# Optimization experiments

Measured on AMD Instinct MI355X. Metric: run time of the kernel, lower is better.

The kernel has to match this reference:

```python
import jax, jax.numpy as jnp
import numpy as np

D = 256      # model dim
H = 4        # heads
L = 6        # layers (shared weights)
N = 32768    # neuron dim; per-head hidden = N//H = 8192
VOCAB = 256
B, T = 2, 2048
EPS = 1e-5


def _ln(x):
    # LayerNorm over last dim, no affine (matches nn.LayerNorm(D, elementwise_affine=False))
    m = jnp.mean(x, axis=-1, keepdims=True)
    v = jnp.mean((x - m) ** 2, axis=-1, keepdims=True)
    return (x - m) * jax.lax.rsqrt(v + EPS)


def _rope(x):
    # x: [B, H, T, d]
    d = x.shape[-1]
    t = x.shape[-2]
    inv_freq = 1.0 / (10000.0 ** (jnp.arange(0, d, 2, dtype=jnp.float32) / d))
    freqs = jnp.arange(t, dtype=jnp.float32)[:, None] * inv_freq[None, :]  # [T, d/2]
    emb = jnp.concatenate([freqs, freqs], axis=-1)                          # [T, d]
    x1, x2 = x[..., : d // 2], x[..., d // 2 :]
    x_rot = jnp.concatenate([-x2, x1], axis=-1)
    return x * jnp.cos(emb) + x_rot * jnp.sin(emb)


def _linear_attn(q, k, v):
    # q,k: [B,H,T,n]; v: [B,T,D]. Raw (unnormalized) scores, STRICTLY causal mask
    # (tril with diagonal=-1, i.e. token t attends to s < t only), no softmax.
    qr = _rope(q)
    kr = _rope(k)
    scores = jnp.einsum('bhtn,bhsn->bhts', qr, kr)  # [B,H,T,T]
    t_idx = jnp.arange(q.shape[-2])
    mask = t_idx[:, None] > t_idx[None, :]          # strict lower triangle
    scores = jnp.where(mask, scores, jnp.zeros((), scores.dtype))
    return jnp.einsum('bhts,bsd->bhtd', scores, v)  # [B,H,T,D]


def setup_inputs() -> dict:
    key = jax.random.key(0)
    ks = jax.random.split(key, 6)
    idx = jax.random.randint(ks[0], (B, T), 0, VOCAB, dtype=jnp.int64)
    std = 0.02
    wte = std * jax.random.normal(ks[1], (VOCAB, D), dtype=jnp.float32)
    encoder = std * jax.random.normal(ks[2], (N, D), dtype=jnp.float32)
    decoder_x = std * jax.random.normal(ks[3], (H, D, N // H), dtype=jnp.float32)
    decoder_y = std * jax.random.normal(ks[4], (H, D, N // H), dtype=jnp.float32)
    readout = std * jax.random.normal(ks[5], (D, VOCAB), dtype=jnp.float32)
    return {"idx": idx, "wte": wte, "encoder": encoder,
            "decoder_x": decoder_x, "decoder_y": decoder_y, "readout": readout}


def reference(idx, wte, encoder, decoder_x, decoder_y, readout):
    # Dropout is identity in eval mode.
    v_ast = _ln(wte[idx])  # [B,T,D]
    for _ in range(L):  # weights SHARED across layers
        x = jax.nn.relu(jnp.einsum('btd,hdn->bhtn', v_ast, decoder_x))  # [B,H,T,N/H]
        a_ast = _linear_attn(x, x, v_ast)                               # [B,H,T,D]
        y = jax.nn.relu(jnp.einsum('bhtd,hdn->bhtn', _ln(a_ast), decoder_y)) * x
        y_flat = jnp.transpose(y, (0, 2, 1, 3)).reshape(y.shape[0], y.shape[2], N)  # [B,T,N]
        v_ast = _ln(v_ast + _ln(y_flat @ encoder))
    return v_ast @ readout  # [B,T,VOCAB]
```

## Files before the change

kernel.cpp:

```cpp
#include <hip/hip_runtime.h>
#include <stdint.h>

typedef unsigned short u16;
typedef __bf16 bfv8 __attribute__((ext_vector_type(8)));
typedef float f32x4 __attribute__((ext_vector_type(4)));

#define BM 128
#define BN 128
#define BK 32

__device__ __forceinline__ float b2f(u16 u){ union{float f; unsigned int i;} x; x.i = ((unsigned int)u)<<16; return x.f; }
__device__ __forceinline__ u16 f2b(float f){ union{float f; unsigned int i;} x; x.f = f; unsigned int r = x.i + 0x7fffu + ((x.i>>16)&1u); return (u16)(r>>16); }

__device__ __forceinline__ void load16_lds(const void* g, void* l){
  __builtin_amdgcn_global_load_lds(
      (const __attribute__((address_space(1))) void*)g,
      (__attribute__((address_space(3))) void*)l, 16, 0, 0);
}

__device__ __forceinline__ void swz(int& bx, int& by, int& bz){
  int gx = gridDim.x, gy = gridDim.y;
  int nw = gx*gy*gridDim.z;
  int flat = blockIdx.x + gx*(blockIdx.y + gy*blockIdx.z);
  int q = nw >> 3, r = nw & 7, xcd = flat & 7, i = flat >> 3;
  int wg = (xcd < r ? xcd*(q+1) : r*(q+1) + (xcd-r)*q) + i;
  bx = wg % gx; int t = wg / gx; by = t % gy; bz = t / gy;
}

struct GP {
  const u16* A; const u16* Bt; const u16* A2; const u16* Bt2;
  const u16* ct; const u16* st;
  float* Cf; u16* Cb; u16* Y;
  int bh0, zs, zm;
};

template<int LDA, int LDB, bool PAIRB>
__device__ __forceinline__ void kloop(const u16* A, const u16* Bt, int m0, int n0,
                                      int kbeg, int kend,
                                      u16 (&As)[2][4096], u16 (&Bs)[2][4096],
                                      f32x4 (&acc)[4][4]){
  const int tid = threadIdx.x;
  const int lane = tid & 63;
  const int wid = tid >> 6;
  const int wm = wid >> 1, wn = wid & 1;
  const int srow = tid >> 2, sslot = tid & 3;
  const int nt = (kend - kbeg) / BK;
  if (nt <= 0) return;

  auto stage = [&](int k0, int buf){
    #pragma unroll
    for (int q = 0; q < 2; ++q){
      int row = q*64 + srow;
      int ks = sslot ^ ((row >> 1) & 3);
      load16_lds(A + (long)(m0 + row)*LDA + (k0 + ks*8), &As[buf][q*2048 + wid*512]);
    }
    #pragma unroll
    for (int q = 0; q < 2; ++q){
      int row = q*64 + srow;
      int ks = sslot ^ ((row >> 1) & 3);
      long brow;
      if (PAIRB){ int wnb = row >> 6, sub = (row >> 5) & 1, r5 = row & 31;
                  brow = n0 + wnb*32 + r5 + sub*4096; }
      else brow = n0 + row;
      load16_lds(Bt + brow*(long)LDB + (k0 + ks*8), &Bs[buf][q*2048 + wid*512]);
    }
  };
  auto compute = [&](int buf){
    bfv8 af[4], bf[4];
    const int r16 = lane & 15, s4 = lane >> 4;
    #pragma unroll
    for (int i = 0; i < 4; ++i){
      int ar = wm*64 + i*16 + r16;
      af[i] = *(const bfv8*)(&As[buf][ar*BK + ((s4 ^ ((ar>>1)&3))*8)]);
      int br = wn*64 + i*16 + r16;
      bf[i] = *(const bfv8*)(&Bs[buf][br*BK + ((s4 ^ ((br>>1)&3))*8)]);
    }
    #pragma unroll
    for (int i = 0; i < 4; ++i)
      #pragma unroll
      for (int j = 0; j < 4; ++j)
        acc[i][j] = __builtin_amdgcn_mfma_f32_16x16x32_bf16(af[i], bf[j], acc[i][j], 0,0,0);
  };

  stage(kbeg, 0);
  int cur = 0;
  for (int t = 0; t < nt-1; ++t){
    stage(kbeg + (t+1)*BK, cur^1);
    asm volatile("s_waitcnt vmcnt(4)" ::: "memory");
    __builtin_amdgcn_s_barrier();
    compute(cur);
    asm volatile("s_waitcnt lgkmcnt(0)" ::: "memory");
    __builtin_amdgcn_s_barrier();
    cur ^= 1;
  }
  asm volatile("s_waitcnt vmcnt(0)" ::: "memory");
  __builtin_amdgcn_s_barrier();
  compute(cur);
  asm volatile("s_waitcnt lgkmcnt(0)" ::: "memory");
  __builtin_amdgcn_s_barrier();
}

template<int LDA, int LDB, int PAIR>
__device__ __forceinline__ void kloop256(const u16* A, const u16* Bt, int m0, int n0,
                                         int kbeg, int kend,
                                         u16 (&As)[2][8192], u16 (&Bs)[2][8192],
                                         f32x4 (&acc)[8][4]){
  const int tid = threadIdx.x;
  const int lane = tid & 63;
  const int wid = tid >> 6;
  const int srow = tid >> 2;
  const int sslot = tid & 3;
  const int nt = (kend - kbeg) / BK;
  if (nt <= 0) return;

  auto stage = [&](int k0, int buf){
    #pragma unroll
    for (int q = 0; q < 2; ++q){
      int row = q*128 + srow;
      int ks = sslot ^ ((row >> 1) & 3);
      load16_lds(A + (long)(m0 + row)*LDA + (k0 + ks*8), &As[buf][q*4096 + wid*512]);
    }
    #pragma unroll
    for (int q = 0; q < 2; ++q){
      int row = q*128 + srow;
      int ks = sslot ^ ((row >> 1) & 3);
      long brow;
      if (PAIR) brow = n0 + (row & 127) + (long)(row >> 7)*4096;
      else      brow = n0 + row;
      load16_lds(Bt + brow*(long)LDB + (k0 + ks*8), &Bs[buf][q*4096 + wid*512]);
    }
  };
  auto compute = [&](int buf){
    const int wm = wid >> 2, wn = wid & 3;
    const int r16 = lane & 15, s4 = lane >> 4;
    bfv8 af[8], bf[4];
    #pragma unroll
    for (int i = 0; i < 8; ++i){
      int ar = wm*128 + i*16 + r16;
      af[i] = *(const bfv8*)(&As[buf][ar*BK + ((s4 ^ ((ar>>1)&3))*8)]);
    }
    #pragma unroll
    for (int j = 0; j < 4; ++j){
      int br;
      if (PAIR) br = (j < 2) ? (wn*32 + j*16 + r16) : (128 + wn*32 + (j-2)*16 + r16);
      else      br = wn*64 + j*16 + r16;
      bf[j] = *(const bfv8*)(&Bs[buf][br*BK + ((s4 ^ ((br>>1)&3))*8)]);
    }
    #pragma unroll
    for (int i = 0; i < 8; ++i)
      #pragma unroll
      for (int j = 0; j < 4; ++j)
        acc[i][j] = __builtin_amdgcn_mfma_f32_16x16x32_bf16(af[i], bf[j], acc[i][j], 0,0,0);
  };

  stage(kbeg, 0);
  int cur = 0;
  for (int t = 0; t < nt-1; ++t){
    stage(kbeg + (t+1)*BK, cur^1);
    asm volatile("s_waitcnt vmcnt(4)" ::: "memory");
    __builtin_amdgcn_s_barrier();
    compute(cur);
    asm volatile("s_waitcnt lgkmcnt(0)" ::: "memory");
    __builtin_amdgcn_s_barrier();
    cur ^= 1;
  }
  asm volatile("s_waitcnt vmcnt(0)" ::: "memory");
  __builtin_amdgcn_s_barrier();
  compute(cur);
  asm volatile("s_waitcnt lgkmcnt(0)" ::: "memory");
  __builtin_amdgcn_s_barrier();
}

#define EPI_SETUP const int lane = threadIdx.x & 63, wid = threadIdx.x >> 6; \
  const int wm = wid >> 1, wn = wid & 1; const int r16 = lane & 15, s4 = lane >> 4;
#define EPI_SETUP8 const int lane = threadIdx.x & 63, wid = threadIdx.x >> 6; \
  const int wm = wid >> 2, wn = wid & 3; const int r16 = lane & 15, s4 = lane >> 4;

__global__ __launch_bounds__(512) void g_rope(GP p){
  int bx, by, bz; swz(bx, by, bz);
  const int m0 = by*256, n0 = bx*128, z = bz;
  const int bh = p.bh0 + z, b = bh >> 2, h = bh & 3;
  __shared__ u16 As[2][8192], Bs[2][8192];
  f32x4 acc[8][4] = {};
  kloop256<256,256,1>(p.A + (long)b*524288, p.Bt + (long)h*2097152, m0, n0, 0, 256, As, Bs, acc);
  EPI_SETUP8
  #pragma unroll
  for (int i = 0; i < 8; ++i)
    #pragma unroll
    for (int j = 0; j < 2; ++j){
      int cl = n0 + wn*32 + j*16 + r16;
      #pragma unroll
      for (int v = 0; v < 4; ++v){
        int row = m0 + wm*128 + i*16 + s4*4 + v;
        float x1 = fmaxf(acc[i][j][v], 0.f);
        float x2 = fmaxf(acc[i][j+2][v], 0.f);
        float c = b2f(p.ct[(long)row*4096 + cl]);
        float s = b2f(p.st[(long)row*4096 + cl]);
        p.Cb[(long)z*16777216 + (long)row*8192 + cl]        = f2b(x1*c - x2*s);
        p.Cb[(long)z*16777216 + (long)row*8192 + cl + 4096] = f2b(x2*c + x1*s);
      }
    }
}

__global__ __launch_bounds__(512) void g_qk(GP p){
  int bx, by, bz; swz(bx, by, bz);
  const int m0 = by*256, n0 = bx*256, z = bz;
  if (n0 > m0) return;
  __shared__ u16 As[2][8192], Bs[2][8192];
  f32x4 acc[8][4] = {};
  const u16* A = p.A + (long)z*16777216;
  kloop256<8192,8192,0>(A, A, m0, n0, 0, 8192, As, Bs, acc);
  EPI_SETUP8
  u16* C = p.Cb + (long)z*4194304;
  #pragma unroll
  for (int i = 0; i < 8; ++i)
    #pragma unroll
    for (int j = 0; j < 4; ++j){
      int col = n0 + wn*64 + j*16 + r16;
      #pragma unroll
      for (int v = 0; v < 4; ++v){
        int row = m0 + wm*128 + i*16 + s4*4 + v;
        C[(long)row*2048 + col] = f2b(row > col ? acc[i][j][v] : 0.f);
      }
    }
}

__global__ __launch_bounds__(512) void g_enc(GP p){
  int bx, by, bz; swz(bx, by, bz);
  const int m0 = by*256, sp = bx, head = bz;
  const int h = (p.bh0 + head) & 3;
  const int kbeg = sp*4096, kend = kbeg + 4096;
  __shared__ u16 As[2][8192], Bs[2][8192];
  f32x4 acc[8][4] = {};
  kloop256<8192,32768,0>(p.A + (long)head*16777216, p.Bt + (long)h*8192, m0, 0, kbeg, kend, As, Bs, acc);
  EPI_SETUP8
  float* C = p.Cf + (long)(head*2 + sp)*524288;
  #pragma unroll
  for (int i = 0; i < 8; ++i)
    #pragma unroll
    for (int j = 0; j < 4; ++j){
      int col = wn*64 + j*16 + r16;
      #pragma unroll
      for (int v = 0; v < 4; ++v){
        int row = m0 + wm*128 + i*16 + s4*4 + v;
        C[(long)row*256 + col] = acc[i][j][v];
      }
    }
}

__global__ __launch_bounds__(256) void g_pv(GP p){
  int bx, by, bz; swz(bx, by, bz);
  const int m0 = by*BM, n0 = bx*BN;
  const int head = bz >> p.zs, sl = bz & p.zm;
  const int b = (p.bh0 + head) >> 2;
  const int kc = 2048 >> p.zs;
  const int kbeg = sl*kc;
  const int kend = min(min(2048, m0 + BM), kbeg + kc);
  __shared__ u16 As[2][4096], Bs[2][4096];
  f32x4 acc[4][4] = {};
  kloop<2048,2048,false>(p.A + (long)head*4194304, p.Bt + (long)b*524288, m0, n0, kbeg, kend, As, Bs, acc);
  EPI_SETUP
  #pragma unroll
  for (int i = 0; i < 4; ++i)
    #pragma unroll
    for (int j = 0; j < 4; ++j){
      int col = n0 + wn*64 + j*16 + r16;
      #pragma unroll
      for (int v = 0; v < 4; ++v){
        int row = m0 + wm*64 + i*16 + s4*4 + v;
        p.Cf[(long)bz*524288 + (long)row*256 + col] = acc[i][j][v];
      }
    }
}

__global__ __launch_bounds__(256) void g_fuse(GP p){
  int bx, by, bz; swz(bx, by, bz);
  const int m0 = by*BM, n0 = bx*BN, z = bz;
  const int bh = p.bh0 + z, b = bh >> 2, h = bh & 3;
  __shared__ u16 As[2][4096], Bs[2][4096];
  f32x4 acc1[4][4] = {}, acc2[4][4] = {};
  kloop<256,256,false>(p.A  + (long)z*524288, p.Bt  + (long)h*2097152, m0, n0, 0, 256, As, Bs, acc1);
  kloop<256,256,false>(p.A2 + (long)b*524288, p.Bt2 + (long)h*2097152, m0, n0, 0, 256, As, Bs, acc2);
  EPI_SETUP
  #pragma unroll
  for (int i = 0; i < 4; ++i)
    #pragma unroll
    for (int j = 0; j < 4; ++j){
      int col = n0 + wn*64 + j*16 + r16;
      #pragma unroll
      for (int v = 0; v < 4; ++v){
        int row = m0 + wm*64 + i*16 + s4*4 + v;
        p.Y[(long)z*16777216 + (long)row*8192 + col] =
            f2b(fmaxf(acc1[i][j][v], 0.f) * fmaxf(acc2[i][j][v], 0.f));
      }
    }
}

__global__ __launch_bounds__(256) void g_out(GP p){
  int bx, by, bz; swz(bx, by, bz); (void)bz;
  const int m0 = by*BM, n0 = bx*BN;
  __shared__ u16 As[2][4096], Bs[2][4096];
  f32x4 acc[4][4] = {};
  kloop<256,256,false>(p.A, p.Bt, m0, n0, 0, 256, As, Bs, acc);
  EPI_SETUP
  #pragma unroll
  for (int i = 0; i < 4; ++i)
    #pragma unroll
    for (int j = 0; j < 4; ++j){
      int col = n0 + wn*64 + j*16 + r16;
      #pragma unroll
      for (int v = 0; v < 4; ++v){
        int row = m0 + wm*64 + i*16 + s4*4 + v;
        p.Cf[(long)row*256 + col] = acc[i][j][v];
      }
    }
}


__device__ __forceinline__ float wave_sum(float v){
  #pragma unroll
  for (int o = 32; o > 0; o >>= 1) v += __shfl_down(v, o, 64);
  return v;
}
__device__ __forceinline__ float block_sum(float v, float* sm){
  v = wave_sum(v);
  __syncthreads();
  if ((threadIdx.x & 63) == 0) sm[threadIdx.x >> 6] = v;
  __syncthreads();
  return sm[0] + sm[1] + sm[2] + sm[3];
}

__global__ __launch_bounds__(256) void k_embed(const int* idx, const float* wte,
                                               u16* vbf, u16* vbt){
  __shared__ float sm[4];
  __shared__ int is64_s;
  int row = blockIdx.x, d = threadIdx.x;
  int oddnz = (d < 64) ? (idx[2*d + 1] != 0) : 0;
  unsigned long long mb = __ballot(oddnz);
  if (threadIdx.x == 0) is64_s = (mb == 0ULL);
  __syncthreads();
  int tok = is64_s ? idx[2*row] : idx[row];
  float x = wte[tok*256 + d];
  float m = block_sum(x, sm) * (1.f/256.f);
  float dd = x - m;
  float var = block_sum(dd*dd, sm) * (1.f/256.f);
  float y = dd * rsqrtf(var + 1e-5f);
  vbf[(long)row*256 + d] = f2b(y);
  int b = row >> 11, t = row & 2047;
  vbt[((long)(b*256 + d))*2048 + t] = f2b(y);
}

__global__ __launch_bounds__(256) void k_ln(const float* abuf, u16* out, int pv){
  __shared__ float sm[4];
  int row = blockIdx.x, d = threadIdx.x;
  int head = row >> 11, t = row & 2047;
  float x = 0.f;
  for (int s = 0; s < pv; ++s) x += abuf[((long)(head*pv + s) << 19) + (long)t*256 + d];
  float m = block_sum(x, sm) * (1.f/256.f);
  float dd = x - m;
  float var = block_sum(dd*dd, sm) * (1.f/256.f);
  out[(long)row*256 + d] = f2b(dd * rsqrtf(var + 1e-5f));
}

__global__ __launch_bounds__(256) void k_acc(const float* part, float* t1,
                                             int bh0, int gc, int ps){
  int t = blockIdx.x, d = threadIdx.x;
  long o = (long)t*256 + d;
  float s0 = 0.f, s1 = 0.f;
  for (int z = 0; z < gc; ++z){
    float v = 0.f;
    for (int sp = 0; sp < ps; ++sp) v += part[((long)(z*ps + sp) << 19) + o];
    if (((bh0 + z) >> 2) == 0) s0 += v; else s1 += v;
  }
  #pragma unroll
  for (int b = 0; b < 2; ++b){
    int lo = bh0 > 4*b ? bh0 : 4*b;
    int hi = (bh0 + gc) < (4*b + 4) ? (bh0 + gc) : (4*b + 4);
    if (lo < hi){
      float s = b == 0 ? s0 : s1;
      if (lo == 4*b) t1[((long)b << 19) + o] = s;
      else           t1[((long)b << 19) + o] += s;
    }
  }
}

__global__ __launch_bounds__(256) void k_finish(const float* t1, u16* vbf, u16* vbt){
  __shared__ float sm[4];
  int row = blockIdx.x; int d = threadIdx.x;
  int b = row >> 11, t = row & 2047;
  float s = t1[(long)row*256 + d];
  float m = block_sum(s, sm) * (1.f/256.f);
  float dd = s - m;
  float var = block_sum(dd*dd, sm) * (1.f/256.f);
  float u = dd * rsqrtf(var + 1e-5f);
  float wv = b2f(vbf[(long)row*256 + d]) + u;
  float m2 = block_sum(wv, sm) * (1.f/256.f);
  float d2 = wv - m2;
  float v2 = block_sum(d2*d2, sm) * (1.f/256.f);
  float y = d2 * rsqrtf(v2 + 1e-5f);
  vbf[(long)row*256 + d] = f2b(y);
  vbt[((long)(b*256 + d))*2048 + t] = f2b(y);
}

__global__ __launch_bounds__(256) void k_cossin(u16* ct, u16* st){
  int tid = blockIdx.x*256 + threadIdx.x;
  int t = tid >> 12, i = tid & 4095;
  float f = powf(10000.0f, -(float)i * (1.0f/4096.0f));
  float a = (float)t * f;
  float s, c; sincosf(a, &s, &c);
  ct[tid] = f2b(c); st[tid] = f2b(s);
}

__global__ void k_transpose(const float* in, u16* out, int R, int C, long in_z, long out_z){
  __shared__ float tile[32][33];
  const float* I = in + (long)blockIdx.z * in_z;
  u16* O = out + (long)blockIdx.z * out_z;
  int c0 = blockIdx.x*32, r0 = blockIdx.y*32;
  int tx = threadIdx.x, ty = threadIdx.y;
  #pragma unroll
  for (int k = 0; k < 4; ++k){ int r = ty + k*8; tile[r][tx] = I[(long)(r0+r)*C + c0+tx]; }
  __syncthreads();
  #pragma unroll
  for (int k = 0; k < 4; ++k){ int r = ty + k*8; O[(long)(c0+r)*R + r0+tx] = f2b(tile[tx][r]); }
}


extern "C" void kernel_launch(void* const* d_in, const int* in_sizes, int n_in,
                              void* d_out, int out_size, void* d_ws, size_t ws_size,
                              hipStream_t stream){
  const int*   idx = (const int*)d_in[0];
  const float* wte = (const float*)d_in[1];
  const float* enc = (const float*)d_in[2];
  const float* dx  = (const float*)d_in[3];
  const float* dy  = (const float*)d_in[4];
  const float* ro  = (const float*)d_in[5];
  float* out = (float*)d_out;
  (void)in_sizes; (void)n_in; (void)out_size;

  int gc = 1, pv = 2;
  {
    const int gcs[4] = {4, 3, 2, 1};
    for (int i = 0; i < 4; ++i){
      int g = gcs[i]; int pvt = (g >= 4) ? 1 : 2;
      size_t need = 92274688UL + (size_t)g*(33554432UL + 8388608UL + (size_t)pvt*2097152UL);
      if (need <= ws_size){ gc = g; pv = pvt; break; }
    }
  }
  const int ps = 2;
  const int pvs = (pv == 2) ? 1 : 0;

  char* w = (char*)d_ws;
  size_t off = 0;
  auto alloc = [&](size_t b){ size_t r = off; off += (b + 255) & ~(size_t)255; return r; };
  u16*   v_bf  = (u16*)  (w + alloc(4096UL*256*2));
  u16*   v_bt  = (u16*)  (w + alloc(2UL*256*2048*2));
  u16*   dxT   = (u16*)  (w + alloc(4UL*8192*256*2));
  u16*   dyT   = (u16*)  (w + alloc(4UL*8192*256*2));
  u16*   encT  = (u16*)  (w + alloc(256UL*32768*2));
  u16*   ct    = (u16*)  (w + alloc(2048UL*4096*2));
  u16*   st    = (u16*)  (w + alloc(2048UL*4096*2));
  float* t1    = (float*)(w + alloc(2UL*2048*256*4));
  u16*   xbuf  = (u16*)  (w + alloc((size_t)gc*33554432));
  u16*   scb   = (u16*)  (w + alloc((size_t)gc*8388608));
  float* abuf  = (float*)(w + alloc((size_t)gc*pv*2097152UL));
  float* part  = (float*)scb;
  u16*   lnAb  = (u16*)((char*)scb + (size_t)gc*ps*2097152UL);
  u16*   roT   = (u16*)t1;

  dim3 tb(32, 8);
  k_cossin<<<32768, 256, 0, stream>>>(ct, st);
  k_transpose<<<dim3(256, 8, 4),  tb, 0, stream>>>(dx,  dxT,  256,   8192, 256L*8192, 8192L*256);
  k_transpose<<<dim3(256, 8, 4),  tb, 0, stream>>>(dy,  dyT,  256,   8192, 256L*8192, 8192L*256);
  k_transpose<<<dim3(8, 1024, 1), tb, 0, stream>>>(enc, encT, 32768, 256,  0, 0);
  k_embed<<<4096, 256, 0, stream>>>(idx, wte, v_bf, v_bt);

  for (int l = 0; l < 6; ++l){
    for (int bh0 = 0; bh0 < 8; bh0 += gc){
      int ze = (8 - bh0 < gc) ? (8 - bh0) : gc;
      { GP g{}; g.bh0=bh0; g.A=v_bf; g.Bt=dxT; g.ct=ct; g.st=st; g.Cb=xbuf;
        g_rope<<<dim3(32,8,ze), 512, 0, stream>>>(g); }
      { GP g{}; g.bh0=bh0; g.A=xbuf; g.Cb=scb;
        g_qk<<<dim3(8,8,ze), 512, 0, stream>>>(g); }
      { GP g{}; g.bh0=bh0; g.A=scb; g.Bt=v_bt; g.Cf=abuf; g.zs=pvs; g.zm=pv-1;
        g_pv<<<dim3(2,16,ze*pv), 256, 0, stream>>>(g); }
      k_ln<<<ze*2048, 256, 0, stream>>>(abuf, lnAb, pv);
      { GP g{}; g.bh0=bh0; g.A=lnAb; g.Bt=dyT; g.A2=v_bf; g.Bt2=dxT; g.Y=xbuf;
        g_fuse<<<dim3(64,16,ze), 256, 0, stream>>>(g); }
      { GP g{}; g.bh0=bh0; g.A=xbuf; g.Bt=encT; g.Cf=part;
        g_enc<<<dim3(ps,8,ze), 512, 0, stream>>>(g); }
      k_acc<<<2048, 256, 0, stream>>>(part, t1, bh0, ze, ps);
    }
    k_finish<<<4096, 256, 0, stream>>>(t1, v_bf, v_bt);
  }
  k_transpose<<<dim3(8, 8, 1), tb, 0, stream>>>(ro, roT, 256, 256, 0, 0);
  { GP g{}; g.A=v_bf; g.Bt=roT; g.Cf=out;
    g_out<<<dim3(2,32,1), 256, 0, stream>>>(g); }
}
```

Before: 8.809 ms.

## Retile GEMM kernels: BK=64 for 128-tiles, 256-tile fuse, 128-tile qk/enc

After: 8.659 ms. Within noise of the previous version (-1.7%).

```diff
diff --git a/kernel.cpp b/kernel.cpp
--- a/kernel.cpp
+++ b/kernel.cpp
@@ -7,7 +7,7 @@
 
 #define BM 128
 #define BN 128
-#define BK 32
+#define BK 64
 
 __device__ __forceinline__ float b2f(u16 u){ union{float f; unsigned int i;} x; x.i = ((unsigned int)u)<<16; return x.f; }
 __device__ __forceinline__ u16 f2b(float f){ union{float f; unsigned int i;} x; x.f = f; unsigned int r = x.i + 0x7fffu + ((x.i>>16)&1u); return (u16)(r>>16); }
@@ -37,27 +37,28 @@
 template<int LDA, int LDB, bool PAIRB>
 __device__ __forceinline__ void kloop(const u16* A, const u16* Bt, int m0, int n0,
                                       int kbeg, int kend,
-                                      u16 (&As)[2][4096], u16 (&Bs)[2][4096],
+                                      u16 (&As)[2][8192], u16 (&Bs)[2][8192],
                                       f32x4 (&acc)[4][4]){
   const int tid = threadIdx.x;
   const int lane = tid & 63;
   const int wid = tid >> 6;
   const int wm = wid >> 1, wn = wid & 1;
-  const int srow = tid >> 2, sslot = tid & 3;
+  const int rr = tid >> 3;
+  const int slot = tid & 7;
   const int nt = (kend - kbeg) / BK;
   if (nt <= 0) return;
 
   auto stage = [&](int k0, int buf){
     #pragma unroll
-    for (int q = 0; q < 2; ++q){
-      int row = q*64 + srow;
-      int ks = sslot ^ ((row >> 1) & 3);
+    for (int q = 0; q < 4; ++q){
+      int row = q*32 + rr;
+      int ks = slot ^ (row & 7);
       load16_lds(A + (long)(m0 + row)*LDA + (k0 + ks*8), &As[buf][q*2048 + wid*512]);
     }
     #pragma unroll
-    for (int q = 0; q < 2; ++q){
-      int row = q*64 + srow;
-      int ks = sslot ^ ((row >> 1) & 3);
+    for (int q = 0; q < 4; ++q){
+      int row = q*32 + rr;
+      int ks = slot ^ (row & 7);
       long brow;
       if (PAIRB){ int wnb = row >> 6, sub = (row >> 5) & 1, r5 = row & 31;
                   brow = n0 + wnb*32 + r5 + sub*4096; }
@@ -66,26 +67,100 @@
     }
   };
   auto compute = [&](int buf){
-    bfv8 af[4], bf[4];
     const int r16 = lane & 15, s4 = lane >> 4;
     #pragma unroll
-    for (int i = 0; i < 4; ++i){
-      int ar = wm*64 + i*16 + r16;
-      af[i] = *(const bfv8*)(&As[buf][ar*BK + ((s4 ^ ((ar>>1)&3))*8)]);
-      int br = wn*64 + i*16 + r16;
-      bf[i] = *(const bfv8*)(&Bs[buf][br*BK + ((s4 ^ ((br>>1)&3))*8)]);
-    }
-    #pragma unroll
-    for (int i = 0; i < 4; ++i)
-      #pragma unroll
-      for (int j = 0; j < 4; ++j)
-        acc[i][j] = __builtin_amdgcn_mfma_f32_16x16x32_bf16(af[i], bf[j], acc[i][j], 0,0,0);
+    for (int kk = 0; kk < 2; ++kk){
+      bfv8 af[4], bf[4];
+      #pragma unroll
+      for (int i = 0; i < 4; ++i){
+        int ar = wm*64 + i*16 + r16;
+        af[i] = *(const bfv8*)(&As[buf][ar*64 + (((kk*4 + s4) ^ (ar & 7))*8)]);
+        int br = wn*64 + i*16 + r16;
+        bf[i] = *(const bfv8*)(&Bs[buf][br*64 + (((kk*4 + s4) ^ (br & 7))*8)]);
+      }
+      #pragma unroll
+      for (int i = 0; i < 4; ++i)
+        #pragma unroll
+        for (int j = 0; j < 4; ++j)
+          acc[i][j] = __builtin_amdgcn_mfma_f32_16x16x32_bf16(af[i], bf[j], acc[i][j], 0,0,0);
+    }
   };
 
   stage(kbeg, 0);
   int cur = 0;
   for (int t = 0; t < nt-1; ++t){
     stage(kbeg + (t+1)*BK, cur^1);
+    asm volatile("s_waitcnt vmcnt(8)" ::: "memory");
+    __builtin_amdgcn_s_barrier();
+    compute(cur);
+    asm volatile("s_waitcnt lgkmcnt(0)" ::: "memory");
+    __builtin_amdgcn_s_barrier();
+    cur ^= 1;
+  }
+  asm volatile("s_waitcnt vmcnt(0)" ::: "memory");
+  __builtin_amdgcn_s_barrier();
+  compute(cur);
+  asm volatile("s_waitcnt lgkmcnt(0)" ::: "memory");
+  __builtin_amdgcn_s_barrier();
+}
+
+template<int LDA, int LDB, int PAIR>
+__device__ __forceinline__ void kloop256(const u16* A, const u16* Bt, int m0, int n0,
+                                         int kbeg, int kend,
+                                         u16 (&As)[2][8192], u16 (&Bs)[2][8192],
+                                         f32x4 (&acc)[8][4]){
+  const int tid = threadIdx.x;
+  const int lane = tid & 63;
+  const int wid = tid >> 6;
+  const int srow = tid >> 2;
+  const int sslot = tid & 3;
+  const int nt = (kend - kbeg) / 32;
+  if (nt <= 0) return;
+
+  auto stage = [&](int k0, int buf){
+    #pragma unroll
+    for (int q = 0; q < 2; ++q){
+      int row = q*128 + srow;
+      int ks = sslot ^ ((row >> 1) & 3);
+      load16_lds(A + (long)(m0 + row)*LDA + (k0 + ks*8), &As[buf][q*4096 + wid*512]);
+    }
+    #pragma unroll
+    for (int q = 0; q < 2; ++q){
+      int row = q*128 + srow;
+      int ks = sslot ^ ((row >> 1) & 3);
+      long brow;
+      if (PAIR) brow = n0 + (row & 127) + (long)(row >> 7)*4096;
+      else      brow = n0 + row;
+      load16_lds(Bt + brow*(long)LDB + (k0 + ks*8), &Bs[buf][q*4096 + wid*512]);
+    }
+  };
+  auto compute = [&](int buf){
+    const int wm = wid >> 2, wn = wid & 3;
+    const int r16 = lane & 15, s4 = lane >> 4;
+    bfv8 af[8], bf[4];
+    #pragma unroll
+    for (int i = 0; i < 8; ++i){
+      int ar = wm*128 + i*16 + r16;
+      af[i] = *(const bfv8*)(&As[buf][ar*32 + ((s4 ^ ((ar>>1)&3))*8)]);
+    }
+    #pragma unroll
+    for (int j = 0; j < 4; ++j){
+      int br;
+      if (PAIR) br = (j < 2) ? (wn*32 + j*16 + r16) : (128 + wn*32 + (j-2)*16 + r16);
+      else      br = wn*64 + j*16 + r16;
+      bf[j] = *(const bfv8*)(&Bs[buf][br*32 + ((s4 ^ ((br>>1)&3))*8)]);
+    }
+    #pragma unroll
+    for (int i = 0; i < 8; ++i)
+      #pragma unroll
+      for (int j = 0; j < 4; ++j)
+        acc[i][j] = __builtin_amdgcn_mfma_f32_16x16x32_bf16(af[i], bf[j], acc[i][j], 0,0,0);
+  };
+
+  stage(kbeg, 0);
+  int cur = 0;
+  for (int t = 0; t < nt-1; ++t){
+    stage(kbeg + (t+1)*32, cur^1);
     asm volatile("s_waitcnt vmcnt(4)" ::: "memory");
     __builtin_amdgcn_s_barrier();
     compute(cur);
@@ -100,77 +175,6 @@
   __builtin_amdgcn_s_barrier();
 }
 
-template<int LDA, int LDB, int PAIR>
-__device__ __forceinline__ void kloop256(const u16* A, const u16* Bt, int m0, int n0,
-                                         int kbeg, int kend,
-                                         u16 (&As)[2][8192], u16 (&Bs)[2][8192],
-                                         f32x4 (&acc)[8][4]){
-  const int tid = threadIdx.x;
-  const int lane = tid & 63;
-  const int wid = tid >> 6;
-  const int srow = tid >> 2;
-  const int sslot = tid & 3;
-  const int nt = (kend - kbeg) / BK;
-  if (nt <= 0) return;
-
-  auto stage = [&](int k0, int buf){
-    #pragma unroll
-    for (int q = 0; q < 2; ++q){
-      int row = q*128 + srow;
-      int ks = sslot ^ ((row >> 1) & 3);
-      load16_lds(A + (long)(m0 + row)*LDA + (k0 + ks*8), &As[buf][q*4096 + wid*512]);
-    }
-    #pragma unroll
-    for (int q = 0; q < 2; ++q){
-      int row = q*128 + srow;
-      int ks = sslot ^ ((row >> 1) & 3);
-      long brow;
-      if (PAIR) brow = n0 + (row & 127) + (long)(row >> 7)*4096;
-      else      brow = n0 + row;
-      load16_lds(Bt + brow*(long)LDB + (k0 + ks*8), &Bs[buf][q*4096 + wid*512]);
-    }
-  };
-  auto compute = [&](int buf){
-    const int wm = wid >> 2, wn = wid & 3;
-    const int r16 = lane & 15, s4 = lane >> 4;
-    bfv8 af[8], bf[4];
-    #pragma unroll
-    for (int i = 0; i < 8; ++i){
-      int ar = wm*128 + i*16 + r16;
-      af[i] = *(const bfv8*)(&As[buf][ar*BK + ((s4 ^ ((ar>>1)&3))*8)]);
-    }
-    #pragma unroll
-    for (int j = 0; j < 4; ++j){
-      int br;
-      if (PAIR) br = (j < 2) ? (wn*32 + j*16 + r16) : (128 + wn*32 + (j-2)*16 + r16);
-      else      br = wn*64 + j*16 + r16;
-      bf[j] = *(const bfv8*)(&Bs[buf][br*BK + ((s4 ^ ((br>>1)&3))*8)]);
-    }
-    #pragma unroll
-    for (int i = 0; i < 8; ++i)
-      #pragma unroll
-      for (int j = 0; j < 4; ++j)
-        acc[i][j] = __builtin_amdgcn_mfma_f32_16x16x32_bf16(af[i], bf[j], acc[i][j], 0,0,0);
-  };
-
-  stage(kbeg, 0);
-  int cur = 0;
-  for (int t = 0; t < nt-1; ++t){
-    stage(kbeg + (t+1)*BK, cur^1);
-    asm volatile("s_waitcnt vmcnt(4)" ::: "memory");
-    __builtin_amdgcn_s_barrier();
-    compute(cur);
-    asm volatile("s_waitcnt lgkmcnt(0)" ::: "memory");
-    __builtin_amdgcn_s_barrier();
-    cur ^= 1;
-  }
-  asm volatile("s_waitcnt vmcnt(0)" ::: "memory");
-  __builtin_amdgcn_s_barrier();
-  compute(cur);
-  asm volatile("s_waitcnt lgkmcnt(0)" ::: "memory");
-  __builtin_amdgcn_s_barrier();
-}
-
 #define EPI_SETUP const int lane = threadIdx.x & 63, wid = threadIdx.x >> 6; \
   const int wm = wid >> 1, wn = wid & 1; const int r16 = lane & 15, s4 = lane >> 4;
 #define EPI_SETUP8 const int lane = threadIdx.x & 63, wid = threadIdx.x >> 6; \
@@ -202,48 +206,25 @@
     }
 }
 
-__global__ __launch_bounds__(512) void g_qk(GP p){
+__global__ __launch_bounds__(256) void g_qk(GP p){
   int bx, by, bz; swz(bx, by, bz);
-  const int m0 = by*256, n0 = bx*256, z = bz;
-  if (n0 > m0) return;
+  const int m0 = by*BM, n0 = bx*BN, z = bz;
+  if (n0 >= m0 + BM) return;
   __shared__ u16 As[2][8192], Bs[2][8192];
-  f32x4 acc[8][4] = {};
+  f32x4 acc[4][4] = {};
   const u16* A = p.A + (long)z*16777216;
-  kloop256<8192,8192,0>(A, A, m0, n0, 0, 8192, As, Bs, acc);
-  EPI_SETUP8
+  kloop<8192,8192,false>(A, A, m0, n0, 0, 8192, As, Bs, acc);
+  EPI_SETUP
   u16* C = p.Cb + (long)z*4194304;
   #pragma unroll
-  for (int i = 0; i < 8; ++i)
+  for (int i = 0; i < 4; ++i)
     #pragma unroll
     for (int j = 0; j < 4; ++j){
       int col = n0 + wn*64 + j*16 + r16;
       #pragma unroll
       for (int v = 0; v < 4; ++v){
-        int row = m0 + wm*128 + i*16 + s4*4 + v;
+        int row = m0 + wm*64 + i*16 + s4*4 + v;
         C[(long)row*2048 + col] = f2b(row > col ? acc[i][j][v] : 0.f);
-      }
-    }
-}
-
-__global__ __launch_bounds__(512) void g_enc(GP p){
-  int bx, by, bz; swz(bx, by, bz);
-  const int m0 = by*256, sp = bx, head = bz;
-  const int h = (p.bh0 + head) & 3;
-  const int kbeg = sp*4096, kend = kbeg + 4096;
-  __shared__ u16 As[2][8192], Bs[2][8192];
-  f32x4 acc[8][4] = {};
-  kloop256<8192,32768,0>(p.A + (long)head*16777216, p.Bt + (long)h*8192, m0, 0, kbeg, kend, As, Bs, acc);
-  EPI_SETUP8
-  float* C = p.Cf + (long)(head*2 + sp)*524288;
-  #pragma unroll
-  for (int i = 0; i < 8; ++i)
-    #pragma unroll
-    for (int j = 0; j < 4; ++j){
-      int col = wn*64 + j*16 + r16;
-      #pragma unroll
-      for (int v = 0; v < 4; ++v){
-        int row = m0 + wm*128 + i*16 + s4*4 + v;
-        C[(long)row*256 + col] = acc[i][j][v];
       }
     }
 }
@@ -256,7 +237,7 @@
   const int kc = 2048 >> p.zs;
   const int kbeg = sl*kc;
   const int kend = min(min(2048, m0 + BM), kbeg + kc);
-  __shared__ u16 As[2][4096], Bs[2][4096];
+  __shared__ u16 As[2][8192], Bs[2][8192];
   f32x4 acc[4][4] = {};
   kloop<2048,2048,false>(p.A + (long)head*4194304, p.Bt + (long)b*524288, m0, n0, kbeg, kend, As, Bs, acc);
   EPI_SETUP
@@ -273,14 +254,49 @@
     }
 }
 
-__global__ __launch_bounds__(256) void g_fuse(GP p){
+__global__ __launch_bounds__(512) void g_fuse(GP p){
   int bx, by, bz; swz(bx, by, bz);
-  const int m0 = by*BM, n0 = bx*BN, z = bz;
+  const int m0 = by*256, n0 = bx*256, z = bz;
   const int bh = p.bh0 + z, b = bh >> 2, h = bh & 3;
-  __shared__ u16 As[2][4096], Bs[2][4096];
-  f32x4 acc1[4][4] = {}, acc2[4][4] = {};
-  kloop<256,256,false>(p.A  + (long)z*524288, p.Bt  + (long)h*2097152, m0, n0, 0, 256, As, Bs, acc1);
-  kloop<256,256,false>(p.A2 + (long)b*524288, p.Bt2 + (long)h*2097152, m0, n0, 0, 256, As, Bs, acc2);
+  __shared__ u16 As[2][8192], Bs[2][8192];
+  f32x4 acc[8][4] = {};
+  kloop256<256,256,0>(p.A + (long)z*524288, p.Bt + (long)h*2097152, m0, n0, 0, 256, As, Bs, acc);
+  unsigned stash[8][4][2];
+  #pragma unroll
+  for (int i = 0; i < 8; ++i)
+    #pragma unroll
+    for (int j = 0; j < 4; ++j){
+      stash[i][j][0] = (unsigned)f2b(fmaxf(acc[i][j][0],0.f)) | ((unsigned)f2b(fmaxf(acc[i][j][1],0.f)) << 16);
+      stash[i][j][1] = (unsigned)f2b(fmaxf(acc[i][j][2],0.f)) | ((unsigned)f2b(fmaxf(acc[i][j][3],0.f)) << 16);
+      acc[i][j] = f32x4{0.f,0.f,0.f,0.f};
+    }
+  kloop256<256,256,0>(p.A2 + (long)b*524288, p.Bt2 + (long)h*2097152, m0, n0, 0, 256, As, Bs, acc);
+  EPI_SETUP8
+  #pragma unroll
+  for (int i = 0; i < 8; ++i)
+    #pragma unroll
+    for (int j = 0; j < 4; ++j){
+      int col = n0 + wn*64 + j*16 + r16;
+      #pragma unroll
+      for (int v = 0; v < 4; ++v){
+        int row = m0 + wm*128 + i*16 + s4*4 + v;
+        float y1 = b2f((u16)((stash[i][j][v>>1] >> ((v&1)*16)) & 0xffffu));
+        p.Y[(long)z*16777216 + (long)row*8192 + col] =
+            f2b(fmaxf(acc[i][j][v], 0.f) * y1);
+      }
+    }
+}
+
+__global__ __launch_bounds__(256) void g_enc(GP p){
+  int bx, by, bz; swz(bx, by, bz);
+  const int m0 = by*BM, n0 = bx*BN;
+  const int head = bz >> p.zs, sp = bz & p.zm;
+  const int h = (p.bh0 + head) & 3;
+  const int kc = 8192 >> p.zs;
+  const int kbeg = sp*kc, kend = kbeg + kc;
+  __shared__ u16 As[2][8192], Bs[2][8192];
+  f32x4 acc[4][4] = {};
+  kloop<8192,32768,false>(p.A + (long)head*16777216, p.Bt + (long)h*8192, m0, n0, kbeg, kend, As, Bs, acc);
   EPI_SETUP
   #pragma unroll
   for (int i = 0; i < 4; ++i)
@@ -290,8 +306,7 @@
       #pragma unroll
       for (int v = 0; v < 4; ++v){
         int row = m0 + wm*64 + i*16 + s4*4 + v;
-        p.Y[(long)z*16777216 + (long)row*8192 + col] =
-            f2b(fmaxf(acc1[i][j][v], 0.f) * fmaxf(acc2[i][j][v], 0.f));
+        p.Cf[(long)bz*524288 + (long)row*256 + col] = acc[i][j][v];
       }
     }
 }
@@ -299,7 +314,7 @@
 __global__ __launch_bounds__(256) void g_out(GP p){
   int bx, by, bz; swz(bx, by, bz); (void)bz;
   const int m0 = by*BM, n0 = bx*BN;
-  __shared__ u16 As[2][4096], Bs[2][4096];
+  __shared__ u16 As[2][8192], Bs[2][8192];
   f32x4 acc[4][4] = {};
   kloop<256,256,false>(p.A, p.Bt, m0, n0, 0, 256, As, Bs, acc);
   EPI_SETUP
@@ -480,14 +495,14 @@
       { GP g{}; g.bh0=bh0; g.A=v_bf; g.Bt=dxT; g.ct=ct; g.st=st; g.Cb=xbuf;
         g_rope<<<dim3(32,8,ze), 512, 0, stream>>>(g); }
       { GP g{}; g.bh0=bh0; g.A=xbuf; g.Cb=scb;
-        g_qk<<<dim3(8,8,ze), 512, 0, stream>>>(g); }
+        g_qk<<<dim3(16,16,ze), 256, 0, stream>>>(g); }
       { GP g{}; g.bh0=bh0; g.A=scb; g.Bt=v_bt; g.Cf=abuf; g.zs=pvs; g.zm=pv-1;
         g_pv<<<dim3(2,16,ze*pv), 256, 0, stream>>>(g); }
       k_ln<<<ze*2048, 256, 0, stream>>>(abuf, lnAb, pv);
       { GP g{}; g.bh0=bh0; g.A=lnAb; g.Bt=dyT; g.A2=v_bf; g.Bt2=dxT; g.Y=xbuf;
-        g_fuse<<<dim3(64,16,ze), 256, 0, stream>>>(g); }
-      { GP g{}; g.bh0=bh0; g.A=xbuf; g.Bt=encT; g.Cf=part;
-        g_enc<<<dim3(ps,8,ze), 512, 0, stream>>>(g); }
+        g_fuse<<<dim3(32,8,ze), 512, 0, stream>>>(g); }
+      { GP g{}; g.bh0=bh0; g.A=xbuf; g.Bt=encT; g.Cf=part; g.zs=1; g.zm=1;
+        g_enc<<<dim3(2,16,ze*ps), 256, 0, stream>>>(g); }
       k_acc<<<2048, 256, 0, stream>>>(part, t1, bh0, ze, ps);
     }
     k_finish<<<4096, 256, 0, stream>>>(t1, v_bf, v_bt);
```
